# Performance work log

Hardware: AMD Instinct MI355X
Metric: run time of the kernel (lower is better)

The kernel has to match this reference:

```python
import jax, jax.numpy as jnp
import numpy as np

N_NODES = 50000
N_EDGES = 800000
D_NODE = 128      # n_in_node_props
D_EDGE = 32       # n_in_edge_props
L_EDGE = 16       # n_latent_edges
L_NODE = 64       # n_latent_nodes
D_OUT = 128       # n_out_node_props


def setup_inputs() -> dict:
    key = jax.random.key(0)
    ks = jax.random.split(key, 8)
    x = jax.random.normal(ks[0], (N_NODES, D_NODE), dtype=jnp.float32)
    edge_index = jax.random.randint(ks[1], (2, N_EDGES), 0, N_NODES, dtype=jnp.int64)
    edge_attr = jax.random.normal(ks[2], (N_EDGES, D_EDGE), dtype=jnp.float32)
    W_gcn = jax.random.normal(ks[3], (D_NODE, L_NODE), dtype=jnp.float32) * (1.0 / np.sqrt(D_NODE))
    b_gcn = jnp.zeros((L_NODE,), dtype=jnp.float32)
    W_edge = jax.random.normal(ks[4], (D_EDGE, L_EDGE), dtype=jnp.float32) * (1.0 / np.sqrt(D_EDGE))
    b_edge = jnp.zeros((L_EDGE,), dtype=jnp.float32)
    W_node = jax.random.normal(ks[5], (L_EDGE * L_NODE, D_OUT), dtype=jnp.float32) * (1.0 / np.sqrt(L_EDGE * L_NODE))
    b_node = jnp.zeros((D_OUT,), dtype=jnp.float32)
    return {"x": x, "edge_index": edge_index, "edge_attr": edge_attr,
            "W_gcn": W_gcn, "b_gcn": b_gcn, "W_edge": W_edge, "b_edge": b_edge,
            "W_node": W_node, "b_node": b_node}


def reference(x, edge_index, edge_attr, W_gcn, b_gcn, W_edge, b_edge, W_node, b_node):
    """LatentGraph forward: per-latent-channel GCNConv (with self-loops and
    symmetric normalization, PyG semantics) followed by an MLP over the
    concatenated channel outputs."""
    N = x.shape[0]
    # edge latent weights: [E, L], ReLU ensures non-negative edge weights
    edge_props = jax.nn.relu(edge_attr @ W_edge + b_edge)
    # shared GCN linear transform of node features: [N, C]
    xW = x @ W_gcn
    # add self loops (weight 1) once; reused by every channel
    loop = jnp.arange(N)
    row = jnp.concatenate([edge_index[0], loop])  # source (message origin)
    col = jnp.concatenate([edge_index[1], loop])  # target (aggregation)

    def one_channel(carry, w):  # w: [E] latent edge weights for this channel
        wf = jnp.concatenate([w, jnp.ones((N,), w.dtype)])  # [E+N]
        deg = jax.ops.segment_sum(wf, col, num_segments=N)  # weighted in-degree
        dinv = jnp.where(deg > 0, jax.lax.rsqrt(deg), 0.0)
        norm = dinv[row] * wf * dinv[col]                   # [E+N]
        out = jax.ops.segment_sum(norm[:, None] * xW[row], col, num_segments=N)
        return carry, out + b_gcn                            # [N, C]

    _, outs = jax.lax.scan(one_channel, None, edge_props.T)  # [L, N, C]
    # concat over channels in loop order -> [N, L*C]
    feats = jnp.transpose(outs, (1, 0, 2)).reshape(N, L_EDGE * L_NODE)
    return jax.nn.relu(feats @ W_node + b_node)  # y: [N, D_OUT]
```

## Files before the change

kernel.cpp:

```cpp
#include <hip/hip_runtime.h>
#include <hip/hip_fp16.h>

typedef _Float16 f16x8 __attribute__((ext_vector_type(8)));
typedef float f32x4 __attribute__((ext_vector_type(4)));
typedef unsigned u32x4 __attribute__((ext_vector_type(4)));
typedef unsigned short u16;

#define DN 128
#define DE 32
#define LE 16
#define LN 64
#define DOUT 128
#define ST 1032

__device__ inline u16 f2h(float f) { return __half_as_ushort(__float2half(f)); }
__device__ inline float h2f(u16 u) { return __half2float(__ushort_as_half(u)); }
__device__ inline unsigned pack2h(float lo, float hi) {
  return (unsigned)f2h(lo) | ((unsigned)f2h(hi) << 16);
}
__device__ inline void unp2(unsigned u, float& a, float& b) {
  __half2 p = *reinterpret_cast<__half2*>(&u);
  a = __half2float(__low2half(p));
  b = __half2float(__high2half(p));
}
__device__ inline __half2 u2h2(unsigned u) {
  return *reinterpret_cast<__half2*>(&u);
}
__device__ inline unsigned h22u(__half2 h) {
  return *reinterpret_cast<unsigned*>(&h);
}
__device__ inline unsigned hmulu(u16 a, u16 b) {
  return (unsigned)__half_as_ushort(__hmul(__ushort_as_half(a), __ushort_as_half(b)));
}

__device__ inline void packb_one(const float* __restrict__ W, u16* __restrict__ Bp,
                                 int idx, int K, int NCOL) {
  int KT = K >> 5;
  int lane = idx & 63;
  int rest = idx >> 6;
  int kt = rest % KT, nt = rest / KT;
  int col = nt * 16 + (lane & 15);
  int kb = kt * 32 + (lane >> 4) * 8;
  u16* dst = Bp + (size_t)idx * 8;
#pragma unroll
  for (int i = 0; i < 8; ++i) dst[i] = f2h(W[(size_t)(kb + i) * NCOL + col]);
}

__global__ __launch_bounds__(256) void k_count(const int* __restrict__ ei,
    int* __restrict__ cnt, int* __restrict__ rank, int E) {
  int e = blockIdx.x * 256 + threadIdx.x;
  if (e < E) rank[e] = atomicAdd(&cnt[ei[E + e]], 1);
}

__global__ __launch_bounds__(1024) void k_scan_packb(const int* __restrict__ cnt,
    int* __restrict__ offs, int N,
    const float* __restrict__ Wg, u16* __restrict__ WgP,
    const float* __restrict__ Wn, u16* __restrict__ WnP) {
  const int totA = (DN / 32) * (LN / 16) * 64;
  const int totB = ((LE * LN) / 32) * (DOUT / 16) * 64;
  if (blockIdx.x != 0) {
    int idx = (blockIdx.x - 1) * 1024 + threadIdx.x;
    if (idx < totA) packb_one(Wg, WgP, idx, DN, LN);
    else if (idx < totA + totB) packb_one(Wn, WnP, idx - totA, LE * LN, DOUT);
    return;
  }
  __shared__ int wsum[16];
  int t = threadIdx.x;
  int chunk = (N + 1023) >> 10;
  int s0 = t * chunk;
  int s1 = min(s0 + chunk, N);
  int s = 0;
  for (int i = s0; i < s1; ++i) s += cnt[i];
  int lane = t & 63, wid = t >> 6;
  int v = s;
#pragma unroll
  for (int d = 1; d < 64; d <<= 1) {
    int u = __shfl_up(v, d);
    if (lane >= d) v += u;
  }
  if (lane == 63) wsum[wid] = v;
  __syncthreads();
  if (t == 0) {
    int run = 0;
    for (int w = 0; w < 16; ++w) { int xv = wsum[w]; wsum[w] = run; run += xv; }
  }
  __syncthreads();
  int run = v - s + wsum[wid];
  for (int i = s0; i < s1; ++i) { offs[i] = run; run += cnt[i]; }
  if (s1 == N && s0 < N) offs[N] = run;
}

template <int K, int NCOL, int MT, bool FIN, bool AF32, bool OUT16>
__device__ inline void gemm_body(int bid, const void* __restrict__ Av,
    const u16* __restrict__ Bp, const float* __restrict__ bias,
    void* __restrict__ outv, int M) {
  constexpr int NT = NCOL / 16;
  constexpr int KT = K / 32;
  const u16* A16 = (const u16*)Av;
  const float* A32 = (const float*)Av;
  int lane = threadIdx.x & 63;
  int wid = threadIdx.x >> 6;
  int m0 = bid * (MT * 64) + wid * (MT * 16);
  f32x4 acc[MT][NT];
#pragma unroll
  for (int mt = 0; mt < MT; ++mt)
#pragma unroll
    for (int nt = 0; nt < NT; ++nt) {
      acc[mt][nt][0] = 0.f; acc[mt][nt][1] = 0.f;
      acc[mt][nt][2] = 0.f; acc[mt][nt][3] = 0.f;
    }
  int rr[MT]; bool vv[MT];
#pragma unroll
  for (int mt = 0; mt < MT; ++mt) {
    rr[mt] = m0 + mt * 16 + (lane & 15);
    vv[mt] = rr[mt] < M;
  }
  int ko = (lane >> 4) * 8;
#pragma unroll 8
  for (int kt = 0; kt < KT; ++kt) {
    f16x8 a[MT];
#pragma unroll
    for (int mt = 0; mt < MT; ++mt) {
#pragma unroll
      for (int i = 0; i < 8; ++i) a[mt][i] = (_Float16)0.f;
      if constexpr (AF32) {
        if (vv[mt]) {
          const float4* p4 = (const float4*)(A32 + (size_t)rr[mt] * K + ko + kt * 32);
          float4 u0 = p4[0], u1 = p4[1];
          a[mt][0]=(_Float16)u0.x; a[mt][1]=(_Float16)u0.y;
          a[mt][2]=(_Float16)u0.z; a[mt][3]=(_Float16)u0.w;
          a[mt][4]=(_Float16)u1.x; a[mt][5]=(_Float16)u1.y;
          a[mt][6]=(_Float16)u1.z; a[mt][7]=(_Float16)u1.w;
        }
      } else {
        if (vv[mt]) a[mt] = *(const f16x8*)(A16 + (size_t)rr[mt] * K + ko + kt * 32);
      }
    }
#pragma unroll
    for (int nt = 0; nt < NT; ++nt) {
      f16x8 b = *(const f16x8*)(Bp + ((size_t)(nt * KT + kt) * 64 + lane) * 8);
#pragma unroll
      for (int mt = 0; mt < MT; ++mt)
        acc[mt][nt] = __builtin_amdgcn_mfma_f32_16x16x32_f16(a[mt], b, acc[mt][nt], 0, 0, 0);
    }
  }
  int col0 = lane & 15;
#pragma unroll
  for (int mt = 0; mt < MT; ++mt) {
    int rb = m0 + mt * 16 + ((lane >> 4) << 2);
#pragma unroll
    for (int nt = 0; nt < NT; ++nt) {
      int c = nt * 16 + col0;
      float bb = FIN ? bias[c] : 0.f;
#pragma unroll
      for (int r = 0; r < 4; ++r) {
        int row = rb + r;
        if (row < M) {
          float vvv = acc[mt][nt][r] + bb;
          if (FIN) vvv = fmaxf(vvv, 0.f);
          if constexpr (OUT16) ((u16*)outv)[(size_t)row * NCOL + c] = f2h(vvv);
          else ((float*)outv)[(size_t)row * NCOL + c] = vvv;
        }
      }
    }
  }
}

__global__ __launch_bounds__(256) void k_fill_gemm1(const float* __restrict__ ea,
    const float* __restrict__ We, const float* __restrict__ be,
    const int* __restrict__ ei, const int* __restrict__ rank,
    const int* __restrict__ offs,
    int* __restrict__ src, u16* __restrict__ wh, int E,
    const float* __restrict__ x, const u16* __restrict__ WgP,
    u16* __restrict__ xwh, int N, int GB) {
  int bid = blockIdx.x;
  int g = bid / 5;
  if ((bid % 5 == 0) && g < GB) {
    gemm_body<DN, LN, 1, false, true, true>(g, x, WgP, nullptr, xwh, N);
    return;
  }
  int ngem = min((bid + 4) / 5, GB);
  int e = (bid - ngem) * 256 + threadIdx.x;
  if (e >= E) return;
  const float4* a4 = (const float4*)(ea + (size_t)e * DE);
  float a[DE];
#pragma unroll
  for (int j = 0; j < DE / 4; ++j) {
    float4 v = a4[j];
    a[4*j] = v.x; a[4*j+1] = v.y; a[4*j+2] = v.z; a[4*j+3] = v.w;
  }
  float acc[LE];
#pragma unroll
  for (int l = 0; l < LE; ++l) acc[l] = be[l];
#pragma unroll
  for (int k = 0; k < DE; ++k) {
    float av = a[k];
#pragma unroll
    for (int l = 0; l < LE; ++l) acc[l] = fmaf(av, We[k * LE + l], acc[l]);
  }
  uint4 o0, o1;
  o0.x = pack2h(fmaxf(acc[0], 0.f), fmaxf(acc[1], 0.f));
  o0.y = pack2h(fmaxf(acc[2], 0.f), fmaxf(acc[3], 0.f));
  o0.z = pack2h(fmaxf(acc[4], 0.f), fmaxf(acc[5], 0.f));
  o0.w = pack2h(fmaxf(acc[6], 0.f), fmaxf(acc[7], 0.f));
  o1.x = pack2h(fmaxf(acc[8], 0.f), fmaxf(acc[9], 0.f));
  o1.y = pack2h(fmaxf(acc[10], 0.f), fmaxf(acc[11], 0.f));
  o1.z = pack2h(fmaxf(acc[12], 0.f), fmaxf(acc[13], 0.f));
  o1.w = pack2h(fmaxf(acc[14], 0.f), fmaxf(acc[15], 0.f));
  int c = ei[E + e];
  int pos = offs[c] + rank[e];
  src[pos] = ei[e];
  uint4* o4 = (uint4*)(wh + (size_t)pos * LE);
  o4[0] = o0; o4[1] = o1;
}

__global__ __launch_bounds__(256) void k_dinv(const u16* __restrict__ wh,
    const int* __restrict__ offs, u16* __restrict__ dinvh, int N) {
  int t = threadIdx.x;
  int n = blockIdx.x * 16 + (t >> 4);
  int l = t & 15;
  if (n >= N) return;
  int i0 = offs[n], i1 = offs[n + 1];
  float s = 1.0f;
  for (int i = i0; i < i1; ++i) s += h2f(wh[(size_t)i * LE + l]);
  dinvh[(size_t)n * LE + l] = f2h(rsqrtf(s));
}

__device__ inline void lds_epilogue(int n, int r, int l, int colb, const __half2* acc,
    const u16* __restrict__ dinvh, const u16* __restrict__ xwh,
    const float* __restrict__ bgcn, u16* __restrict__ S) {
  float dn = h2f(dinvh[(size_t)n * LE + l]);
  float dn2 = dn * dn;
  const u32x4* xs4 = (const u32x4*)(xwh + (size_t)n * LN + colb);
  u32x4 m0 = xs4[0], m1 = xs4[1];
  const f32x4* bgp = (const f32x4*)(bgcn + colb);
  f32x4 b0 = bgp[0], b1 = bgp[1], b2 = bgp[2], b3 = bgp[3];
  float xv[16];
  unp2(m0[0], xv[0], xv[1]);   unp2(m0[1], xv[2], xv[3]);
  unp2(m0[2], xv[4], xv[5]);   unp2(m0[3], xv[6], xv[7]);
  unp2(m1[0], xv[8], xv[9]);   unp2(m1[1], xv[10], xv[11]);
  unp2(m1[2], xv[12], xv[13]); unp2(m1[3], xv[14], xv[15]);
  float av[16];
  unp2(h22u(acc[0]), av[0], av[1]);   unp2(h22u(acc[1]), av[2], av[3]);
  unp2(h22u(acc[2]), av[4], av[5]);   unp2(h22u(acc[3]), av[6], av[7]);
  unp2(h22u(acc[4]), av[8], av[9]);   unp2(h22u(acc[5]), av[10], av[11]);
  unp2(h22u(acc[6]), av[12], av[13]); unp2(h22u(acc[7]), av[14], av[15]);
  float bgv[16] = {b0[0],b0[1],b0[2],b0[3],b1[0],b1[1],b1[2],b1[3],
                   b2[0],b2[1],b2[2],b2[3],b3[0],b3[1],b3[2],b3[3]};
  float ov[16];
#pragma unroll
  for (int j = 0; j < 16; ++j) ov[j] = bgv[j] + dn * av[j] + dn2 * xv[j];
  u32x4 o0, o1;
  o0[0] = pack2h(ov[0], ov[1]);   o0[1] = pack2h(ov[2], ov[3]);
  o0[2] = pack2h(ov[4], ov[5]);   o0[3] = pack2h(ov[6], ov[7]);
  o1[0] = pack2h(ov[8], ov[9]);   o1[1] = pack2h(ov[10], ov[11]);
  o1[2] = pack2h(ov[12], ov[13]); o1[3] = pack2h(ov[14], ov[15]);
  int off = l * 128 + colb * 2;
  int swz = (l & 7) << 4;
  char* rowp = (char*)(S + (size_t)r * ST);
  *(u32x4*)(rowp + (off ^ swz)) = o0;
  *(u32x4*)(rowp + ((off + 16) ^ swz)) = o1;
}

__global__ __launch_bounds__(512) void k_mega(const int* __restrict__ src,
    const u16* __restrict__ wh, const u16* __restrict__ dinvh,
    const u16* __restrict__ xwh, const float* __restrict__ bgcn,
    const int* __restrict__ offs, const u16* __restrict__ WnP,
    const float* __restrict__ bn, float* __restrict__ y, int N) {
  __shared__ u16 S[16 * ST];
  int tid = threadIdx.x;
  int w = tid >> 6, lane = tid & 63;
  int l = lane & 15, g = lane >> 4;
  int colb = g * 16;
  int nblk = blockIdx.x * 16;
  int r0 = w * 2;
  int n0 = nblk + r0, n1 = n0 + 1;
  bool v0 = n0 < N, v1 = n1 < N;
  const u16* xb = xwh + colb;
  __half2 accA[8], accB[8];
#pragma unroll
  for (int j = 0; j < 8; ++j) { accA[j] = u2h2(0u); accB[j] = u2h2(0u); }
  int iA = v0 ? offs[n0] : 0, eA = v0 ? offs[n0 + 1] : 0;
  int iB = v1 ? offs[n1] : 0, eB = v1 ? offs[n1 + 1] : 0;
  int sA = (iA < eA) ? src[iA] : 0;
  int sB = (iB < eB) ? src[iB] : 0;
  while (iA < eA || iB < eB) {
    bool aA = iA < eA, aB = iB < eB;
    u16 wA = 0, dA = 0, wB = 0, dB = 0;
    u32x4 rA0 = {0,0,0,0}, rA1 = {0,0,0,0}, rB0 = {0,0,0,0}, rB1 = {0,0,0,0};
    int sAn = sA, sBn = sB;
    if (aA) {
      wA = wh[(size_t)iA * LE + l];
      dA = dinvh[(size_t)sA * LE + l];
      const u32x4* q = (const u32x4*)(xb + (size_t)sA * LN);
      rA0 = q[0]; rA1 = q[1];
      if (iA + 1 < eA) sAn = src[iA + 1];
    }
    if (aB) {
      wB = wh[(size_t)iB * LE + l];
      dB = dinvh[(size_t)sB * LE + l];
      const u32x4* q = (const u32x4*)(xb + (size_t)sB * LN);
      rB0 = q[0]; rB1 = q[1];
      if (iB + 1 < eB) sBn = src[iB + 1];
    }
    unsigned cAu = hmulu(wA, dA);
    unsigned cBu = hmulu(wB, dB);
    __half2 ca = u2h2(cAu | (cAu << 16));
    __half2 cb = u2h2(cBu | (cBu << 16));
    accA[0] = __hfma2(ca, u2h2(rA0[0]), accA[0]);
    accA[1] = __hfma2(ca, u2h2(rA0[1]), accA[1]);
    accA[2] = __hfma2(ca, u2h2(rA0[2]), accA[2]);
    accA[3] = __hfma2(ca, u2h2(rA0[3]), accA[3]);
    accA[4] = __hfma2(ca, u2h2(rA1[0]), accA[4]);
    accA[5] = __hfma2(ca, u2h2(rA1[1]), accA[5]);
    accA[6] = __hfma2(ca, u2h2(rA1[2]), accA[6]);
    accA[7] = __hfma2(ca, u2h2(rA1[3]), accA[7]);
    accB[0] = __hfma2(cb, u2h2(rB0[0]), accB[0]);
    accB[1] = __hfma2(cb, u2h2(rB0[1]), accB[1]);
    accB[2] = __hfma2(cb, u2h2(rB0[2]), accB[2]);
    accB[3] = __hfma2(cb, u2h2(rB0[3]), accB[3]);
    accB[4] = __hfma2(cb, u2h2(rB1[0]), accB[4]);
    accB[5] = __hfma2(cb, u2h2(rB1[1]), accB[5]);
    accB[6] = __hfma2(cb, u2h2(rB1[2]), accB[6]);
    accB[7] = __hfma2(cb, u2h2(rB1[3]), accB[7]);
    sA = sAn; sB = sBn;
    iA += aA ? 1 : 0;
    iB += aB ? 1 : 0;
  }
  if (v0) lds_epilogue(n0, r0, l, colb, accA, dinvh, xwh, bgcn, S);
  if (v1) lds_epilogue(n1, r0 + 1, l, colb, accB, dinvh, xwh, bgcn, S);
  __syncthreads();
  f32x4 acc2;
  acc2[0] = 0.f; acc2[1] = 0.f; acc2[2] = 0.f; acc2[3] = 0.f;
  const char* arow = (const char*)(S + (size_t)(lane & 15) * ST);
#pragma unroll 8
  for (int kt = 0; kt < 32; ++kt) {
    int aoff = kt * 64 + g * 16;
    int key = ((aoff >> 7) & 7) << 4;
    f16x8 a = *(const f16x8*)(arow + (aoff ^ key));
    f16x8 b = *(const f16x8*)(WnP + ((size_t)(w * 32 + kt) * 64 + lane) * 8);
    acc2 = __builtin_amdgcn_mfma_f32_16x16x32_f16(a, b, acc2, 0, 0, 0);
  }
  int col = w * 16 + (lane & 15);
  float bb = bn[col];
  int rb = (lane >> 4) * 4;
#pragma unroll
  for (int r = 0; r < 4; ++r) {
    int row = nblk + rb + r;
    if (row < N) y[(size_t)row * DOUT + col] = fmaxf(acc2[r] + bb, 0.f);
  }
}

extern "C" void kernel_launch(void* const* d_in, const int* in_sizes, int n_in,
                              void* d_out, int out_size, void* d_ws, size_t ws_size,
                              hipStream_t stream) {
  const float* x  = (const float*)d_in[0];
  const int*   ei = (const int*)d_in[1];
  const float* ea = (const float*)d_in[2];
  const float* Wg = (const float*)d_in[3];
  const float* bg = (const float*)d_in[4];
  const float* We = (const float*)d_in[5];
  const float* be = (const float*)d_in[6];
  const float* Wn = (const float*)d_in[7];
  const float* bn = (const float*)d_in[8];
  float* outp = (float*)d_out;
  int N = in_sizes[0] / DN;
  int E = in_sizes[1] / 2;

  char* p = (char*)d_ws;
  auto carve = [&](size_t bytes) {
    char* r = p;
    p += (bytes + 255) & ~(size_t)255;
    return (void*)r;
  };
  u16*   wh    = (u16*)carve((size_t)E * LE * 2);
  u16*   xwh   = (u16*)carve((size_t)N * LN * 2);
  u16*   dinvh = (u16*)carve((size_t)N * LE * 2);
  u16*   WnP   = (u16*)carve((size_t)(LE * LN) * DOUT * 2);
  u16*   WgP   = (u16*)carve((size_t)DN * LN * 2);
  int*   offs  = (int*)carve((size_t)(N + 1) * 4);
  int*   cnt   = (int*)carve((size_t)N * 4);
  int*   rank  = (int*)carve((size_t)E * 4);
  int*   src   = (int*)carve((size_t)E * 4);

  hipMemsetAsync(cnt, 0, (size_t)N * 4, stream);

  k_count<<<(E + 255) / 256, 256, 0, stream>>>(ei, cnt, rank, E);
  k_scan_packb<<<18, 1024, 0, stream>>>(cnt, offs, N, Wg, WgP, Wn, WnP);
  int FB = (E + 255) / 256, GB = (N + 63) / 64;
  k_fill_gemm1<<<FB + GB, 256, 0, stream>>>(ea, We, be, ei, rank, offs,
                                            src, wh, E, x, WgP, xwh, N, GB);
  k_dinv<<<(N + 15) / 16, 256, 0, stream>>>(wh, offs, dinvh, N);
  k_mega<<<(N + 15) / 16, 512, 0, stream>>>(src, wh, dinvh, xwh, bg, offs, WnP, bn, outp, N);
}
```

Before: 299.5 us.

## Balance edge aggregation across warps with edge-range split and LDS CAS accumulation

Replaces the fixed two-nodes-per-warp edge loop with an even split of the block's CSR edge range across the 8 warps, so high-degree nodes no longer leave other warps idle. Each warp folds the destination dinv into the per-edge coefficient and adds partial sums into the shared tile with half2 CAS loops. The self-loop and bias term is written first by calling the epilogue with zero accumulators. This adds LDS atomic contention and retry cost at node boundaries, and changes fp16 rounding order.

Result: slower. 311.2 us (+3.9%).

```diff
diff --git a/kernel.cpp b/kernel.cpp
--- a/kernel.cpp
+++ b/kernel.cpp
@@ -29,8 +29,10 @@
 __device__ inline unsigned h22u(__half2 h) {
   return *reinterpret_cast<unsigned*>(&h);
 }
-__device__ inline unsigned hmulu(u16 a, u16 b) {
-  return (unsigned)__half_as_ushort(__hmul(__ushort_as_half(a), __ushort_as_half(b)));
+__device__ inline u16 hmul3(u16 a, u16 b, u16 c) {
+  __half t = __hmul(__hmul(__ushort_as_half(a), __ushort_as_half(b)),
+                    __ushort_as_half(c));
+  return __half_as_ushort(t);
 }
 
 __device__ inline void packb_one(const float* __restrict__ W, u16* __restrict__ Bp,
@@ -262,6 +264,27 @@
   *(u32x4*)(rowp + ((off + 16) ^ swz)) = o1;
 }
 
+__device__ inline void cas_add_u32(unsigned* p, __half2 v) {
+  unsigned cur = *(volatile unsigned*)p;
+  unsigned assumed;
+  do {
+    assumed = cur;
+    __half2 nw = __hadd2(u2h2(assumed), v);
+    cur = atomicCAS(p, assumed, h22u(nw));
+  } while (cur != assumed);
+}
+__device__ inline void lds_cas_add(u16* S, int r, int l, int colb, const __half2* acc) {
+  char* rowp = (char*)(S + (size_t)r * ST);
+  int off = l * 128 + colb * 2;
+  int swz = (l & 7) << 4;
+  unsigned* b0 = (unsigned*)(rowp + (off ^ swz));
+  unsigned* b1 = (unsigned*)(rowp + ((off + 16) ^ swz));
+#pragma unroll
+  for (int j = 0; j < 4; ++j) cas_add_u32(b0 + j, acc[j]);
+#pragma unroll
+  for (int j = 0; j < 4; ++j) cas_add_u32(b1 + j, acc[4 + j]);
+}
+
 __global__ __launch_bounds__(512) void k_mega(const int* __restrict__ src,
     const u16* __restrict__ wh, const u16* __restrict__ dinvh,
     const u16* __restrict__ xwh, const float* __restrict__ bgcn,
@@ -273,62 +296,91 @@
   int l = lane & 15, g = lane >> 4;
   int colb = g * 16;
   int nblk = blockIdx.x * 16;
-  int r0 = w * 2;
-  int n0 = nblk + r0, n1 = n0 + 1;
-  bool v0 = n0 < N, v1 = n1 < N;
-  const u16* xb = xwh + colb;
-  __half2 accA[8], accB[8];
-#pragma unroll
-  for (int j = 0; j < 8; ++j) { accA[j] = u2h2(0u); accB[j] = u2h2(0u); }
-  int iA = v0 ? offs[n0] : 0, eA = v0 ? offs[n0 + 1] : 0;
-  int iB = v1 ? offs[n1] : 0, eB = v1 ? offs[n1 + 1] : 0;
-  int sA = (iA < eA) ? src[iA] : 0;
-  int sB = (iB < eB) ? src[iB] : 0;
-  while (iA < eA || iB < eB) {
-    bool aA = iA < eA, aB = iB < eB;
-    u16 wA = 0, dA = 0, wB = 0, dB = 0;
-    u32x4 rA0 = {0,0,0,0}, rA1 = {0,0,0,0}, rB0 = {0,0,0,0}, rB1 = {0,0,0,0};
-    int sAn = sA, sBn = sB;
-    if (aA) {
-      wA = wh[(size_t)iA * LE + l];
-      dA = dinvh[(size_t)sA * LE + l];
-      const u32x4* q = (const u32x4*)(xb + (size_t)sA * LN);
-      rA0 = q[0]; rA1 = q[1];
-      if (iA + 1 < eA) sAn = src[iA + 1];
+  __half2 acc[8];
+#pragma unroll
+  for (int j = 0; j < 8; ++j) acc[j] = u2h2(0u);
+  {
+    int r0 = 2 * w;
+    int n0 = nblk + r0, n1 = n0 + 1;
+    if (n0 < N) lds_epilogue(n0, r0, l, colb, acc, dinvh, xwh, bgcn, S);
+    if (n1 < N) lds_epilogue(n1, r0 + 1, l, colb, acc, dinvh, xwh, bgcn, S);
+  }
+  __syncthreads();
+  int nEnd = min(nblk + 16, N);
+  if (nblk < N) {
+    int E0 = offs[nblk], E1 = offs[nEnd];
+    int total = E1 - E0;
+    int W = (total + 7) >> 3;
+    int i = E0 + w * W;
+    int iend = min(i + W, E1);
+    if (i < iend) {
+      int n = nblk;
+      int nb = offs[n + 1];
+      while (nb <= i) { ++n; nb = offs[n + 1]; }
+      u16 dnl = dinvh[(size_t)n * LE + l];
+      const u16* xb = xwh + colb;
+      while (i < iend) {
+        if (i >= nb) {
+          lds_cas_add(S, n - nblk, l, colb, acc);
+#pragma unroll
+          for (int j = 0; j < 8; ++j) acc[j] = u2h2(0u);
+          ++n; nb = offs[n + 1];
+          dnl = dinvh[(size_t)n * LE + l];
+          continue;
+        }
+        int lim = min(iend, nb);
+        if (i + 1 < lim) {
+          int s0 = src[i], s1 = src[i + 1];
+          u16 w0 = wh[(size_t)i * LE + l];
+          u16 w1 = wh[(size_t)(i + 1) * LE + l];
+          u16 d0 = dinvh[(size_t)s0 * LE + l];
+          u16 d1 = dinvh[(size_t)s1 * LE + l];
+          const u32x4* p0 = (const u32x4*)(xb + (size_t)s0 * LN);
+          const u32x4* p1 = (const u32x4*)(xb + (size_t)s1 * LN);
+          u32x4 r0a = p0[0], r0b = p0[1];
+          u32x4 r1a = p1[0], r1b = p1[1];
+          unsigned c0 = (unsigned)hmul3(w0, d0, dnl); c0 |= c0 << 16;
+          unsigned c1 = (unsigned)hmul3(w1, d1, dnl); c1 |= c1 << 16;
+          __half2 ch0 = u2h2(c0), ch1 = u2h2(c1);
+          acc[0] = __hfma2(ch0, u2h2(r0a[0]), acc[0]);
+          acc[1] = __hfma2(ch0, u2h2(r0a[1]), acc[1]);
+          acc[2] = __hfma2(ch0, u2h2(r0a[2]), acc[2]);
+          acc[3] = __hfma2(ch0, u2h2(r0a[3]), acc[3]);
+          acc[4] = __hfma2(ch0, u2h2(r0b[0]), acc[4]);
+          acc[5] = __hfma2(ch0, u2h2(r0b[1]), acc[5]);
+          acc[6] = __hfma2(ch0, u2h2(r0b[2]), acc[6]);
+          acc[7] = __hfma2(ch0, u2h2(r0b[3]), acc[7]);
+          acc[0] = __hfma2(ch1, u2h2(r1a[0]), acc[0]);
+          acc[1] = __hfma2(ch1, u2h2(r1a[1]), acc[1]);
+          acc[2] = __hfma2(ch1, u2h2(r1a[2]), acc[2]);
+          acc[3] = __hfma2(ch1, u2h2(r1a[3]), acc[3]);
+          acc[4] = __hfma2(ch1, u2h2(r1b[0]), acc[4]);
+          acc[5] = __hfma2(ch1, u2h2(r1b[1]), acc[5]);
+          acc[6] = __hfma2(ch1, u2h2(r1b[2]), acc[6]);
+          acc[7] = __hfma2(ch1, u2h2(r1b[3]), acc[7]);
+          i += 2;
+        } else {
+          int s0 = src[i];
+          u16 w0 = wh[(size_t)i * LE + l];
+          u16 d0 = dinvh[(size_t)s0 * LE + l];
+          const u32x4* p0 = (const u32x4*)(xb + (size_t)s0 * LN);
+          u32x4 r0a = p0[0], r0b = p0[1];
+          unsigned c0 = (unsigned)hmul3(w0, d0, dnl); c0 |= c0 << 16;
+          __half2 ch0 = u2h2(c0);
+          acc[0] = __hfma2(ch0, u2h2(r0a[0]), acc[0]);
+          acc[1] = __hfma2(ch0, u2h2(r0a[1]), acc[1]);
+          acc[2] = __hfma2(ch0, u2h2(r0a[2]), acc[2]);
+          acc[3] = __hfma2(ch0, u2h2(r0a[3]), acc[3]);
+          acc[4] = __hfma2(ch0, u2h2(r0b[0]), acc[4]);
+          acc[5] = __hfma2(ch0, u2h2(r0b[1]), acc[5]);
+          acc[6] = __hfma2(ch0, u2h2(r0b[2]), acc[6]);
+          acc[7] = __hfma2(ch0, u2h2(r0b[3]), acc[7]);
+          i += 1;
+        }
+      }
+      lds_cas_add(S, n - nblk, l, colb, acc);
     }
-    if (aB) {
-      wB = wh[(size_t)iB * LE + l];
-      dB = dinvh[(size_t)sB * LE + l];
-      const u32x4* q = (const u32x4*)(xb + (size_t)sB * LN);
-      rB0 = q[0]; rB1 = q[1];
-      if (iB + 1 < eB) sBn = src[iB + 1];
-    }
-    unsigned cAu = hmulu(wA, dA);
-    unsigned cBu = hmulu(wB, dB);
-    __half2 ca = u2h2(cAu | (cAu << 16));
-    __half2 cb = u2h2(cBu | (cBu << 16));
-    accA[0] = __hfma2(ca, u2h2(rA0[0]), accA[0]);
-    accA[1] = __hfma2(ca, u2h2(rA0[1]), accA[1]);
-    accA[2] = __hfma2(ca, u2h2(rA0[2]), accA[2]);
-    accA[3] = __hfma2(ca, u2h2(rA0[3]), accA[3]);
-    accA[4] = __hfma2(ca, u2h2(rA1[0]), accA[4]);
-    accA[5] = __hfma2(ca, u2h2(rA1[1]), accA[5]);
-    accA[6] = __hfma2(ca, u2h2(rA1[2]), accA[6]);
-    accA[7] = __hfma2(ca, u2h2(rA1[3]), accA[7]);
-    accB[0] = __hfma2(cb, u2h2(rB0[0]), accB[0]);
-    accB[1] = __hfma2(cb, u2h2(rB0[1]), accB[1]);
-    accB[2] = __hfma2(cb, u2h2(rB0[2]), accB[2]);
-    accB[3] = __hfma2(cb, u2h2(rB0[3]), accB[3]);
-    accB[4] = __hfma2(cb, u2h2(rB1[0]), accB[4]);
-    accB[5] = __hfma2(cb, u2h2(rB1[1]), accB[5]);
-    accB[6] = __hfma2(cb, u2h2(rB1[2]), accB[6]);
-    accB[7] = __hfma2(cb, u2h2(rB1[3]), accB[7]);
-    sA = sAn; sB = sBn;
-    iA += aA ? 1 : 0;
-    iB += aB ? 1 : 0;
-  }
-  if (v0) lds_epilogue(n0, r0, l, colb, accA, dinvh, xwh, bgcn, S);
-  if (v1) lds_epilogue(n1, r0 + 1, l, colb, accB, dinvh, xwh, bgcn, S);
+  }
   __syncthreads();
   f32x4 acc2;
   acc2[0] = 0.f; acc2[1] = 0.f; acc2[2] = 0.f; acc2[3] = 0.f;
```
